# Kernel tuning notes

Measured on AMD Instinct MI355X. Metric: run time of the kernel, lower is better.

## Reference

```python
import jax, jax.numpy as jnp
import numpy as np

DIM = 512
HEADS = 8
DHEAD = 64
B, H, W = 4, 128, 128


def _dwconv(x, k):
    # x: (b, c, h, w), k: (c, 1, 3, 3) depthwise kernel (groups = c)
    return jax.lax.conv_general_dilated(
        x, k, window_strides=(1, 1), padding='SAME',
        dimension_numbers=('NCHW', 'OIHW', 'NCHW'),
        feature_group_count=x.shape[1])


def _l2norm(x, eps=1e-12):
    # torch F.normalize(p=2, dim=-1): x / clamp(||x||, eps)
    n = jnp.sqrt(jnp.sum(x * x, axis=-1, keepdims=True))
    return x / jnp.maximum(n, eps)


def setup_inputs() -> dict:
    key = jax.random.key(0)
    ks = jax.random.split(key, 10)
    s = 0.02
    return {
        'x_in': jax.random.normal(ks[0], (B, H, W, DIM), jnp.float32),
        'illu_fea_trans': jax.random.uniform(ks[1], (B, H, W, DIM), jnp.float32),
        'Wq': jax.random.normal(ks[2], (DIM, DIM), jnp.float32) * s,  # (out,in), no bias
        'Wk': jax.random.normal(ks[3], (DIM, DIM), jnp.float32) * s,
        'Wv': jax.random.normal(ks[4], (DIM, DIM), jnp.float32) * s,
        'rescale': jnp.ones((HEADS, 1, 1), jnp.float32),
        'Wp': jax.random.normal(ks[5], (DIM, DIM), jnp.float32) * s,  # proj weight (out,in)
        'bp': jnp.zeros((DIM,), jnp.float32),
        'pe1': jax.random.normal(ks[6], (DIM, 1, 3, 3), jnp.float32) * s,  # depthwise conv kernels
        'pe2': jax.random.normal(ks[7], (DIM, 1, 3, 3), jnp.float32) * s,
    }


def reference(x_in, illu_fea_trans, Wq, Wk, Wv, rescale, Wp, bp, pe1, pe2):
    b, h, w, c = x_in.shape
    n = h * w
    x = x_in.reshape(b, n, c)
    illu = illu_fea_trans.reshape(b, n, c)

    q = x @ Wq.T
    k = x @ Wk.T
    v = x @ Wv.T

    def to_heads_dn(t):  # (b, n, heads*d) -> (b, heads, d, n)
        return t.reshape(b, n, HEADS, DHEAD).transpose(0, 2, 3, 1)

    illu_h = illu.reshape(b, n, HEADS, DHEAD)
    v = ((v.reshape(b, n, HEADS, DHEAD)) * illu_h).transpose(0, 2, 3, 1)  # (b,heads,d,n)
    q = _l2norm(to_heads_dn(q))  # normalize along n
    k = _l2norm(to_heads_dn(k))

    # channel attention: (b,heads,d,d) score matrix
    attn = jnp.einsum('bhdn,bhen->bhde', k, q) * rescale
    attn = jax.nn.softmax(attn, axis=-1)
    xo = jnp.einsum('bhde,bhen->bhdn', attn, v)  # (b,heads,d,n)

    xo = xo.transpose(0, 3, 1, 2).reshape(b, n, HEADS * DHEAD)  # (b,n,c)
    out_c = (xo @ Wp.T + bp).reshape(b, h, w, c)

    # positional branch: depthwise conv -> GELU -> depthwise conv on v image
    v_img = v.reshape(b, HEADS * DHEAD, h, w)
    p = _dwconv(v_img, pe1)
    p = jax.nn.gelu(p, approximate=False)  # torch F.gelu default = erf
    p = _dwconv(p, pe2)
    out_p = p.transpose(0, 2, 3, 1)

    return out_c + out_p
```

## Files before the change

### kernel.cpp

```cpp
#include <hip/hip_runtime.h>
#include <hip/hip_bf16.h>
#include <math.h>

typedef __bf16 bf16;
typedef __attribute__((ext_vector_type(4))) __bf16 bf16x4;
typedef __attribute__((ext_vector_type(8))) __bf16 bf16x8;
typedef __attribute__((ext_vector_type(4))) float f32x4;

#define GLL(gp, lp) __builtin_amdgcn_global_load_lds( \
    (const __attribute__((address_space(1))) unsigned int*)(gp), \
    (__attribute__((address_space(3))) unsigned int*)(lp), 16, 0, 0)

#define WAIT_LGKM0() do { asm volatile("s_waitcnt lgkmcnt(0)" ::: "memory"); \
                          __builtin_amdgcn_sched_barrier(0); } while (0)
#define WAIT_VMC(n) do { asm volatile("s_waitcnt vmcnt(" #n ")" ::: "memory"); \
                         __builtin_amdgcn_sched_barrier(0); } while (0)
#define BARRIER_FENCE() asm volatile("s_barrier" ::: "memory")


__device__ __forceinline__ bf16x8 cvt8(float4 a, float4 b) {
  bf16x8 o;
  o[0] = (bf16)a.x; o[1] = (bf16)a.y; o[2] = (bf16)a.z; o[3] = (bf16)a.w;
  o[4] = (bf16)b.x; o[5] = (bf16)b.y; o[6] = (bf16)b.z; o[7] = (bf16)b.w;
  return o;
}

__global__ __launch_bounds__(256) void prep_kernel(
    const float* __restrict__ x, const float* __restrict__ Wq,
    const float* __restrict__ Wk, const float* __restrict__ Wv,
    bf16* __restrict__ xb, bf16* __restrict__ wqkv,
    float* __restrict__ zattn, float* __restrict__ ssq, float* __restrict__ ssk)
{
  const long XG = 33554432L / 8;
  const long WG = 262144L / 8;
  long i = (long)blockIdx.x * 256 + threadIdx.x;
  if (i < XG) {
    const float4* xp = (const float4*)x;
    float4 a = xp[i * 2], b = xp[i * 2 + 1];
    *(bf16x8*)(xb + i * 8) = cvt8(a, b);
  } else if (i < XG + 3 * WG) {
    long j = i - XG;
    int w = (int)(j / WG);
    long r = j % WG;
    const float* src = (w == 0) ? Wq : ((w == 1) ? Wk : Wv);
    const float4* sp = (const float4*)src;
    float4 a = sp[r * 2], b = sp[r * 2 + 1];
    *(bf16x8*)(wqkv + (long)w * 262144 + r * 8) = cvt8(a, b);
  } else {
    long j = (i - XG - 3 * WG) * 8;
    float4 z = make_float4(0.f, 0.f, 0.f, 0.f);
    if (j < 131072) {
      *(float4*)(zattn + j) = z; *(float4*)(zattn + j + 4) = z;
    } else if (j < 133120) {
      long r = j - 131072; *(float4*)(ssq + r) = z; *(float4*)(ssq + r + 4) = z;
    } else {
      long r = j - 133120; *(float4*)(ssk + r) = z; *(float4*)(ssk + r + 4) = z;
    }
  }
}

__device__ __forceinline__ void gemm_tile_mainloop(
    const bf16* __restrict__ A, const bf16* __restrict__ B,
    int m0, int n0, bf16* As, bf16* Bs, f32x4 acc[4][4])
{
  int tid = threadIdx.x;
  int lane = tid & 63, wave = tid >> 6;
  int wy = wave >> 1, wx = wave & 1;
  int srow = tid >> 2;
  int scol = ((tid & 3) ^ (srow & 3)) * 8;
  const bf16* ag = A + ((size_t)(m0 + srow) << 9) + scol;
  const bf16* bg = B + ((size_t)(n0 + srow) << 9) + scol;
  bf16* lA = As + wave * 512;
  bf16* lB = Bs + wave * 512;
  int mloc = lane & 15;
  int kq = lane >> 4;

#define STG(t) do { \
    GLL(ag + (t) * 32,         lA + ((t) % 3) * 4096);        \
    GLL(ag + (t) * 32 + 32768, lA + ((t) % 3) * 4096 + 2048); \
    GLL(bg + (t) * 32,         lB + ((t) % 3) * 4096);        \
    GLL(bg + (t) * 32 + 32768, lB + ((t) % 3) * 4096 + 2048); \
  } while (0)

  STG(0);
  STG(1);
  WAIT_VMC(4);
  BARRIER_FENCE();

#pragma unroll
  for (int t = 0; t < 16; ++t) {
    if (t + 2 < 16) STG(t + 2);
    const bf16* Ac = As + (t % 3) * 4096;
    const bf16* Bc = Bs + (t % 3) * 4096;
    bf16x8 af[4], bfr[4];
#pragma unroll
    for (int tt = 0; tt < 4; tt++) {
      int arow = wy * 64 + tt * 16 + mloc;
      af[tt] = *(const bf16x8*)&Ac[arow * 32 + ((kq ^ (arow & 3)) << 3)];
      int brow = wx * 64 + tt * 16 + mloc;
      bfr[tt] = *(const bf16x8*)&Bc[brow * 32 + ((kq ^ (brow & 3)) << 3)];
    }
    WAIT_LGKM0();
    __builtin_amdgcn_s_setprio(1);
#pragma unroll
    for (int ty = 0; ty < 4; ty++)
#pragma unroll
      for (int tx = 0; tx < 4; tx++)
        acc[ty][tx] = __builtin_amdgcn_mfma_f32_16x16x32_bf16(
            af[ty], bfr[tx], acc[ty][tx], 0, 0, 0);
    __builtin_amdgcn_s_setprio(0);
    if (t <= 13)      { WAIT_VMC(4); }
    else if (t == 14) { WAIT_VMC(0); }
    if (t < 15) BARRIER_FENCE();
  }
#undef STG
}

__global__ __launch_bounds__(256, 3) void gemm_qkv_kernel(
    const bf16* __restrict__ xb, const bf16* __restrict__ wqkv,
    const float* __restrict__ illu,
    bf16* __restrict__ qbT, bf16* __restrict__ kbT, bf16* __restrict__ vb,
    float* __restrict__ ssq, float* __restrict__ ssk)
{
  __shared__ __align__(16) bf16 As[12288];
  __shared__ __align__(16) bf16 Bs[12288];
  int bid = blockIdx.x;
  int xcd = bid & 7, s = bid >> 3;
  int mt = xcd * 64 + s / 12, nt = s % 12;
  int m0 = mt * 128, n0 = nt * 128;
  f32x4 acc[4][4] = {};
  gemm_tile_mainloop(xb, wqkv, m0, n0, As, Bs, acc);

  int tid = threadIdx.x, lane = tid & 63, wave = tid >> 6;
  int wy = wave >> 1, wx = wave & 1;
  int r0 = m0 + wy * 64 + ((lane >> 4) << 2);
  int c0 = n0 + wx * 64 + (lane & 15);
  int region = n0 >> 9;
  if (region < 2) {
    bf16* outp = region ? kbT : qbT;
    float* dst = (region ? ssk : ssq) + (m0 >> 14) * 512;
    int bb = r0 >> 14;
    int nl0 = r0 & 16383;
#pragma unroll
    for (int tx = 0; tx < 4; tx++) {
      int lc = (c0 + tx * 16) & 511;
      bf16* colp = outp + (((size_t)bb << 23) + ((size_t)lc << 14));
      float ss = 0.f;
#pragma unroll
      for (int ty = 0; ty < 4; ty++) {
        f32x4 a = acc[ty][tx];
        ss += a[0] * a[0] + a[1] * a[1] + a[2] * a[2] + a[3] * a[3];
        bf16x4 o;
        o[0] = (bf16)a[0]; o[1] = (bf16)a[1]; o[2] = (bf16)a[2]; o[3] = (bf16)a[3];
        *(bf16x4*)&colp[nl0 + ty * 16] = o;
      }
      ss += __shfl_xor(ss, 16);
      ss += __shfl_xor(ss, 32);
      if ((lane >> 4) == 0) atomicAdd(dst + lc, ss);
    }
  } else {
#pragma unroll
    for (int tx = 0; tx < 4; tx++) {
      int lc = (c0 + tx * 16) & 511;
#pragma unroll
      for (int ty = 0; ty < 4; ty++) {
#pragma unroll
        for (int r = 0; r < 4; r++) {
          size_t idx = ((size_t)(r0 + ty * 16 + r) << 9) + lc;
          vb[idx] = (bf16)(acc[ty][tx][r] * illu[idx]);
        }
      }
    }
  }
}

__global__ __launch_bounds__(256) void attn_dots_kernel(
    const bf16* __restrict__ qbT, const bf16* __restrict__ kbT,
    float* __restrict__ attn)
{
  __shared__ __align__(16) bf16 ks[4][4096];
  __shared__ __align__(16) bf16 qs[4][4096];
  int bh = blockIdx.x, sp = blockIdx.y;
  int b = bh >> 3, h = bh & 7;
  int t = threadIdx.x, lane = t & 63, w = t >> 6;
  size_t base = ((size_t)b << 23) + ((size_t)h << 20);
  int n0 = sp * 1024 + w * 256;
  int srow = lane >> 3;
  int scol = ((lane & 7) ^ (srow & 7)) << 3;
  const bf16* kg = kbT + base + (size_t)srow * 16384 + n0 + scol;
  const bf16* qg = qbT + base + (size_t)srow * 16384 + n0 + scol;
  bf16* lk = &ks[w][0];
  bf16* lq = &qs[w][0];
  int mloc = lane & 15, kq = lane >> 4;
  f32x4 acc[4][4] = {};

  for (int it = 0; it < 4; ++it) {
    WAIT_LGKM0();
#pragma unroll
    for (int i = 0; i < 8; ++i) {
      GLL(kg + it * 64 + (size_t)i * 131072, lk + i * 512);
      GLL(qg + it * 64 + (size_t)i * 131072, lq + i * 512);
    }
    WAIT_VMC(0);
    bf16x8 af[4][2], bfq[4][2];
#pragma unroll
    for (int tt = 0; tt < 4; ++tt) {
      int r = tt * 16 + mloc;
#pragma unroll
      for (int kh = 0; kh < 2; ++kh) {
        int slot = (kh * 4 + kq) ^ (r & 7);
        af[tt][kh]  = *(const bf16x8*)&lk[r * 64 + slot * 8];
        bfq[tt][kh] = *(const bf16x8*)&lq[r * 64 + slot * 8];
      }
    }
#pragma unroll
    for (int kh = 0; kh < 2; ++kh)
#pragma unroll
      for (int ta = 0; ta < 4; ++ta)
#pragma unroll
        for (int tb = 0; tb < 4; ++tb)
          acc[ta][tb] = __builtin_amdgcn_mfma_f32_16x16x32_bf16(
              af[ta][kh], bfq[tb][kh], acc[ta][tb], 0, 0, 0);
  }
  float* ap = attn + ((size_t)bh << 12);
  int rr = (lane >> 4) << 2, cc = lane & 15;
#pragma unroll
  for (int ta = 0; ta < 4; ++ta)
#pragma unroll
    for (int tb = 0; tb < 4; ++tb)
#pragma unroll
      for (int r = 0; r < 4; ++r)
        atomicAdd(&ap[(ta * 16 + rr + r) * 64 + tb * 16 + cc], acc[ta][tb][r]);
}

__global__ __launch_bounds__(64) void softmax_kernel(
    float* __restrict__ attn, const float* __restrict__ ssq,
    const float* __restrict__ ssk, const float* __restrict__ rescale)
{
  int bh = blockIdx.x, d = blockIdx.y;
  int b = bh >> 3, h = bh & 7;
  int e = threadIdx.x;
  float nq = fmaxf(sqrtf(ssq[b * 512 + h * 64 + e]), 1e-12f);
  float nk = fmaxf(sqrtf(ssk[b * 512 + h * 64 + d]), 1e-12f);
  float* ap = attn + ((size_t)bh << 12) + d * 64;
  float v = ap[e] * rescale[h] / (nk * nq);
  float m = v;
  for (int o = 32; o > 0; o >>= 1) m = fmaxf(m, __shfl_xor(m, o));
  float ex = expf(v - m);
  float s = ex;
  for (int o = 32; o > 0; o >>= 1) s += __shfl_xor(s, o);
  ap[e] = ex / s;
}

__global__ __launch_bounds__(256) void weff_kernel(
    const float* __restrict__ attn, const float* __restrict__ Wp,
    bf16* __restrict__ wefT)
{
  int cog = blockIdx.x, h = blockIdx.y, b = blockIdx.z;
  __shared__ float at[4096];
  __shared__ float wp[4096];
  int t = threadIdx.x;
  const float* ap = attn + ((size_t)(b * 8 + h) << 12);
  for (int i = t; i < 4096; i += 256) at[i] = ap[i];
  for (int i = t; i < 4096; i += 256) {
    int r = i >> 6, d = i & 63;
    wp[i] = Wp[((size_t)(cog * 64 + r) << 9) + h * 64 + d];
  }
  __syncthreads();
  int co_l = (t & 15) * 4, e_l = (t >> 4) * 4;
  float acc[16] = {0};
  for (int d = 0; d < 64; d++) {
    float w0 = wp[(co_l + 0) * 64 + d];
    float w1 = wp[(co_l + 1) * 64 + d];
    float w2 = wp[(co_l + 2) * 64 + d];
    float w3 = wp[(co_l + 3) * 64 + d];
    float4 av = *(const float4*)&at[d * 64 + e_l];
    acc[0]  += w0 * av.x; acc[1]  += w0 * av.y; acc[2]  += w0 * av.z; acc[3]  += w0 * av.w;
    acc[4]  += w1 * av.x; acc[5]  += w1 * av.y; acc[6]  += w1 * av.z; acc[7]  += w1 * av.w;
    acc[8]  += w2 * av.x; acc[9]  += w2 * av.y; acc[10] += w2 * av.z; acc[11] += w2 * av.w;
    acc[12] += w3 * av.x; acc[13] += w3 * av.y; acc[14] += w3 * av.z; acc[15] += w3 * av.w;
  }
#pragma unroll
  for (int i = 0; i < 4; i++)
#pragma unroll
    for (int j = 0; j < 4; j++)
      wefT[((size_t)b << 18) + ((size_t)(cog * 64 + co_l + i) << 9) + h * 64 + e_l + j] =
          (bf16)acc[i * 4 + j];
}

__global__ __launch_bounds__(256, 3) void gemm_out_kernel(
    const bf16* __restrict__ vb, const bf16* __restrict__ wefT,
    const float* __restrict__ bp, float* __restrict__ out)
{
  __shared__ __align__(16) bf16 As[12288];
  __shared__ __align__(16) bf16 Bs[12288];
  int b = blockIdx.y;
  int bid = blockIdx.x;
  int xcd = bid & 7, s = bid >> 3;
  int mt = xcd * 16 + (s >> 2), nt = s & 3;
  int m0 = mt * 128, n0 = nt * 128;
  const bf16* A = vb + ((size_t)b << 23);
  const bf16* B = wefT + ((size_t)b << 18);
  f32x4 acc[4][4] = {};
  gemm_tile_mainloop(A, B, m0, n0, As, Bs, acc);

  int tid = threadIdx.x, lane = tid & 63, wave = tid >> 6;
  int wy = wave >> 1, wx = wave & 1;
  int r0 = (b << 14) + m0 + wy * 64 + ((lane >> 4) << 2);
  int c0 = n0 + wx * 64 + (lane & 15);
#pragma unroll
  for (int ty = 0; ty < 4; ty++) {
#pragma unroll
    for (int tx = 0; tx < 4; tx++) {
      int lc = c0 + tx * 16;
      float bias = bp[lc];
#pragma unroll
      for (int r = 0; r < 4; r++) {
        int grow = r0 + ty * 16 + r;
        out[((size_t)grow << 9) + lc] = acc[ty][tx][r] + bias;
      }
    }
  }
}

__global__ __launch_bounds__(256) void conv1_kernel(
    const bf16* __restrict__ vb, const float* __restrict__ pe1,
    bf16* __restrict__ pbuf)
{
  int b = blockIdx.y;
  int tile = blockIdx.x;
  int y0 = (tile >> 4) * 8, x0 = (tile & 15) * 8;
  int t = threadIdx.x;
  int cg = (t & 63) * 8, sp0 = t >> 6;
  float w[72];
#pragma unroll
  for (int i = 0; i < 8; i++)
#pragma unroll
    for (int k = 0; k < 9; k++)
      w[i * 9 + k] = pe1[(cg + i) * 9 + k];
  const bf16* vbase = vb + ((size_t)b << 23);
  bf16* pb = pbuf + ((size_t)b << 23);
  for (int s = sp0; s < 64; s += 4) {
    int y = y0 + (s >> 3), x = x0 + (s & 7);
    float a[8] = {0, 0, 0, 0, 0, 0, 0, 0};
#pragma unroll
    for (int ky = 0; ky < 3; ky++) {
      int yy = y + ky - 1;
      if (yy < 0 || yy >= 128) continue;
#pragma unroll
      for (int kx = 0; kx < 3; kx++) {
        int xx = x + kx - 1;
        if (xx < 0 || xx >= 128) continue;
        bf16x8 vv = *(const bf16x8*)&vbase[((size_t)(yy * 128 + xx) << 9) + cg];
#pragma unroll
        for (int i = 0; i < 8; i++) a[i] += (float)vv[i] * w[i * 9 + ky * 3 + kx];
      }
    }
    bf16x8 o;
#pragma unroll
    for (int i = 0; i < 8; i++) {
      float g = 0.5f * a[i] * (1.0f + erff(a[i] * 0.70710678118654752f));
      o[i] = (bf16)g;
    }
    *(bf16x8*)&pb[((size_t)(y * 128 + x) << 9) + cg] = o;
  }
}

__global__ __launch_bounds__(256) void conv2_kernel(
    const bf16* __restrict__ pbuf, const float* __restrict__ pe2,
    float* __restrict__ out)
{
  int b = blockIdx.y;
  int tile = blockIdx.x;
  int y0 = (tile >> 4) * 8, x0 = (tile & 15) * 8;
  int t = threadIdx.x;
  int cg = (t & 63) * 8, sp0 = t >> 6;
  float w[72];
#pragma unroll
  for (int i = 0; i < 8; i++)
#pragma unroll
    for (int k = 0; k < 9; k++)
      w[i * 9 + k] = pe2[(cg + i) * 9 + k];
  const bf16* pb = pbuf + ((size_t)b << 23);
  float* ob = out + ((size_t)b << 23);
  for (int s = sp0; s < 64; s += 4) {
    int y = y0 + (s >> 3), x = x0 + (s & 7);
    float a[8] = {0, 0, 0, 0, 0, 0, 0, 0};
#pragma unroll
    for (int ky = 0; ky < 3; ky++) {
      int yy = y + ky - 1;
      if (yy < 0 || yy >= 128) continue;
#pragma unroll
      for (int kx = 0; kx < 3; kx++) {
        int xx = x + kx - 1;
        if (xx < 0 || xx >= 128) continue;
        bf16x8 vv = *(const bf16x8*)&pb[((size_t)(yy * 128 + xx) << 9) + cg];
#pragma unroll
        for (int i = 0; i < 8; i++) a[i] += (float)vv[i] * w[i * 9 + ky * 3 + kx];
      }
    }
    size_t oi = ((size_t)(y * 128 + x) << 9) + cg;
    float4 o0 = *(float4*)&ob[oi];
    float4 o1 = *(float4*)&ob[oi + 4];
    o0.x += a[0]; o0.y += a[1]; o0.z += a[2]; o0.w += a[3];
    o1.x += a[4]; o1.y += a[5]; o1.z += a[6]; o1.w += a[7];
    *(float4*)&ob[oi] = o0;
    *(float4*)&ob[oi + 4] = o1;
  }
}

extern "C" void kernel_launch(void* const* d_in, const int* in_sizes, int n_in,
                              void* d_out, int out_size, void* d_ws, size_t ws_size,
                              hipStream_t stream) {
  (void)in_sizes; (void)n_in; (void)out_size; (void)ws_size;
  const float* x       = (const float*)d_in[0];
  const float* illu    = (const float*)d_in[1];
  const float* Wq      = (const float*)d_in[2];
  const float* Wk      = (const float*)d_in[3];
  const float* Wv      = (const float*)d_in[4];
  const float* rescale = (const float*)d_in[5];
  const float* Wp      = (const float*)d_in[6];
  const float* bp      = (const float*)d_in[7];
  const float* pe1     = (const float*)d_in[8];
  const float* pe2     = (const float*)d_in[9];
  float* out = (float*)d_out;
  char* ws = (char*)d_ws;

  bf16*  xb   = (bf16*)(ws);
  bf16*  wqkv = (bf16*)(ws + 67108864);
  bf16*  qbT  = (bf16*)(ws + 68681728);
  bf16*  kbT  = (bf16*)(ws + 135790592);
  bf16*  vb   = (bf16*)(ws + 202899456);
  float* ssq  = (float*)(ws + 270008320);
  float* ssk  = (float*)(ws + 270016512);
  float* attn = (float*)(ws + 270024704);
  bf16*  wefT = (bf16*)(ws + 270548992);
  bf16*  pbuf = xb;

  prep_kernel<<<16834, 256, 0, stream>>>(x, Wq, Wk, Wv, xb, wqkv, attn, ssq, ssk);
  gemm_qkv_kernel<<<6144, 256, 0, stream>>>(xb, wqkv, illu, qbT, kbT, vb, ssq, ssk);
  attn_dots_kernel<<<dim3(32, 16), 256, 0, stream>>>(qbT, kbT, attn);
  softmax_kernel<<<dim3(32, 64), 64, 0, stream>>>(attn, ssq, ssk, rescale);
  weff_kernel<<<dim3(8, 8, 4), 256, 0, stream>>>(attn, Wp, wefT);
  gemm_out_kernel<<<dim3(512, 4), 256, 0, stream>>>(vb, wefT, bp, out);
  conv1_kernel<<<dim3(256, 4), 256, 0, stream>>>(vb, pe1, pbuf);
  conv2_kernel<<<dim3(256, 4), 256, 0, stream>>>(pbuf, pe2, out);
}
```

Before: 783.0 us.

## Fuse two depthwise convs via LDS halo tile and change GEMM LDS swizzle

Merges the conv1 (dwconv+GELU) and conv2 kernels into one kernel. Each block computes GELU(conv1) on a 10x10 halo tile for a 128-channel slice, keeps it in shared memory, then applies conv2 from LDS. This removes the round trip of the intermediate bf16 buffer through global memory, at the cost of recomputing halo pixels (about 1.56x conv1 work). It also changes the XOR swizzle in the GEMM mainloop's LDS staging and reads, to use (row>>1)&3 so that LDS bank conflicts drop.

```diff
diff --git a/kernel.cpp b/kernel.cpp
--- a/kernel.cpp
+++ b/kernel.cpp
@@ -67,7 +67,7 @@
   int lane = tid & 63, wave = tid >> 6;
   int wy = wave >> 1, wx = wave & 1;
   int srow = tid >> 2;
-  int scol = ((tid & 3) ^ (srow & 3)) * 8;
+  int scol = ((tid & 3) ^ ((tid >> 3) & 3)) * 8;
   const bf16* ag = A + ((size_t)(m0 + srow) << 9) + scol;
   const bf16* bg = B + ((size_t)(n0 + srow) << 9) + scol;
   bf16* lA = As + wave * 512;
@@ -96,9 +96,9 @@
 #pragma unroll
     for (int tt = 0; tt < 4; tt++) {
       int arow = wy * 64 + tt * 16 + mloc;
-      af[tt] = *(const bf16x8*)&Ac[arow * 32 + ((kq ^ (arow & 3)) << 3)];
+      af[tt] = *(const bf16x8*)&Ac[arow * 32 + ((kq ^ ((arow >> 1) & 3)) << 3)];
       int brow = wx * 64 + tt * 16 + mloc;
-      bfr[tt] = *(const bf16x8*)&Bc[brow * 32 + ((kq ^ (brow & 3)) << 3)];
+      bfr[tt] = *(const bf16x8*)&Bc[brow * 32 + ((kq ^ ((brow >> 1) & 3)) << 3)];
     }
     WAIT_LGKM0();
     __builtin_amdgcn_s_setprio(1);
@@ -323,83 +323,80 @@
   }
 }
 
-__global__ __launch_bounds__(256) void conv1_kernel(
+__global__ __launch_bounds__(256) void conv_fused_kernel(
     const bf16* __restrict__ vb, const float* __restrict__ pe1,
-    bf16* __restrict__ pbuf)
-{
-  int b = blockIdx.y;
+    const float* __restrict__ pe2, float* __restrict__ out)
+{
+  __shared__ __align__(16) bf16 ps[10 * 10 * 128];
+  int b = blockIdx.z;
+  int cs = blockIdx.y;
   int tile = blockIdx.x;
   int y0 = (tile >> 4) * 8, x0 = (tile & 15) * 8;
   int t = threadIdx.x;
-  int cg = (t & 63) * 8, sp0 = t >> 6;
-  float w[72];
+  int cl = (t & 15) * 8;
+  int cg = cs * 128 + cl;
+  int sp = t >> 4;
+  const bf16* vbase = vb + ((size_t)b << 23);
+
+  {
+    float w1[72];
+#pragma unroll
+    for (int i = 0; i < 8; i++)
+#pragma unroll
+      for (int k = 0; k < 9; k++)
+        w1[i * 9 + k] = pe1[(cg + i) * 9 + k];
+    for (int pos = sp; pos < 100; pos += 16) {
+      int py = pos / 10, px = pos % 10;
+      int yy = y0 - 1 + py, xx = x0 - 1 + px;
+      bf16x8 o;
+      if (yy >= 0 && yy < 128 && xx >= 0 && xx < 128) {
+        float a[8] = {0, 0, 0, 0, 0, 0, 0, 0};
+#pragma unroll
+        for (int ky = 0; ky < 3; ky++) {
+          int sy = yy + ky - 1;
+          if (sy < 0 || sy >= 128) continue;
+#pragma unroll
+          for (int kx = 0; kx < 3; kx++) {
+            int sx = xx + kx - 1;
+            if (sx < 0 || sx >= 128) continue;
+            bf16x8 vv = *(const bf16x8*)&vbase[((size_t)(sy * 128 + sx) << 9) + cg];
+#pragma unroll
+            for (int i = 0; i < 8; i++) a[i] += (float)vv[i] * w1[i * 9 + ky * 3 + kx];
+          }
+        }
+#pragma unroll
+        for (int i = 0; i < 8; i++) {
+          float g = 0.5f * a[i] * (1.0f + erff(a[i] * 0.70710678118654752f));
+          o[i] = (bf16)g;
+        }
+      } else {
+#pragma unroll
+        for (int i = 0; i < 8; i++) o[i] = (bf16)0.0f;
+      }
+      *(bf16x8*)&ps[(py * 10 + px) * 128 + cl] = o;
+    }
+  }
+  __syncthreads();
+
+  float w2[72];
 #pragma unroll
   for (int i = 0; i < 8; i++)
 #pragma unroll
     for (int k = 0; k < 9; k++)
-      w[i * 9 + k] = pe1[(cg + i) * 9 + k];
-  const bf16* vbase = vb + ((size_t)b << 23);
-  bf16* pb = pbuf + ((size_t)b << 23);
-  for (int s = sp0; s < 64; s += 4) {
-    int y = y0 + (s >> 3), x = x0 + (s & 7);
+      w2[i * 9 + k] = pe2[(cg + i) * 9 + k];
+  float* ob = out + ((size_t)b << 23);
+  for (int o = sp; o < 64; o += 16) {
+    int oy = o >> 3, ox = o & 7;
     float a[8] = {0, 0, 0, 0, 0, 0, 0, 0};
 #pragma unroll
-    for (int ky = 0; ky < 3; ky++) {
-      int yy = y + ky - 1;
-      if (yy < 0 || yy >= 128) continue;
+    for (int ky = 0; ky < 3; ky++)
 #pragma unroll
       for (int kx = 0; kx < 3; kx++) {
-        int xx = x + kx - 1;
-        if (xx < 0 || xx >= 128) continue;
-        bf16x8 vv = *(const bf16x8*)&vbase[((size_t)(yy * 128 + xx) << 9) + cg];
-#pragma unroll
-        for (int i = 0; i < 8; i++) a[i] += (float)vv[i] * w[i * 9 + ky * 3 + kx];
-      }
-    }
-    bf16x8 o;
-#pragma unroll
-    for (int i = 0; i < 8; i++) {
-      float g = 0.5f * a[i] * (1.0f + erff(a[i] * 0.70710678118654752f));
-      o[i] = (bf16)g;
-    }
-    *(bf16x8*)&pb[((size_t)(y * 128 + x) << 9) + cg] = o;
-  }
-}
-
-__global__ __launch_bounds__(256) void conv2_kernel(
-    const bf16* __restrict__ pbuf, const float* __restrict__ pe2,
-    float* __restrict__ out)
-{
-  int b = blockIdx.y;
-  int tile = blockIdx.x;
-  int y0 = (tile >> 4) * 8, x0 = (tile & 15) * 8;
-  int t = threadIdx.x;
-  int cg = (t & 63) * 8, sp0 = t >> 6;
-  float w[72];
-#pragma unroll
-  for (int i = 0; i < 8; i++)
-#pragma unroll
-    for (int k = 0; k < 9; k++)
-      w[i * 9 + k] = pe2[(cg + i) * 9 + k];
-  const bf16* pb = pbuf + ((size_t)b << 23);
-  float* ob = out + ((size_t)b << 23);
-  for (int s = sp0; s < 64; s += 4) {
-    int y = y0 + (s >> 3), x = x0 + (s & 7);
-    float a[8] = {0, 0, 0, 0, 0, 0, 0, 0};
-#pragma unroll
-    for (int ky = 0; ky < 3; ky++) {
-      int yy = y + ky - 1;
-      if (yy < 0 || yy >= 128) continue;
-#pragma unroll
-      for (int kx = 0; kx < 3; kx++) {
-        int xx = x + kx - 1;
-        if (xx < 0 || xx >= 128) continue;
-        bf16x8 vv = *(const bf16x8*)&pb[((size_t)(yy * 128 + xx) << 9) + cg];
-#pragma unroll
-        for (int i = 0; i < 8; i++) a[i] += (float)vv[i] * w[i * 9 + ky * 3 + kx];
-      }
-    }
-    size_t oi = ((size_t)(y * 128 + x) << 9) + cg;
+        bf16x8 pv = *(const bf16x8*)&ps[((oy + ky) * 10 + (ox + kx)) * 128 + cl];
+#pragma unroll
+        for (int i = 0; i < 8; i++) a[i] += (float)pv[i] * w2[i * 9 + ky * 3 + kx];
+      }
+    size_t oi = ((size_t)((y0 + oy) * 128 + (x0 + ox)) << 9) + cg;
     float4 o0 = *(float4*)&ob[oi];
     float4 o1 = *(float4*)&ob[oi + 4];
     o0.x += a[0]; o0.y += a[1]; o0.z += a[2]; o0.w += a[3];
@@ -435,7 +432,6 @@
   float* ssk  = (float*)(ws + 270016512);
   float* attn = (float*)(ws + 270024704);
   bf16*  wefT = (bf16*)(ws + 270548992);
-  bf16*  pbuf = xb;
 
   prep_kernel<<<16834, 256, 0, stream>>>(x, Wq, Wk, Wv, xb, wqkv, attn, ssq, ssk);
   gemm_qkv_kernel<<<6144, 256, 0, stream>>>(xb, wqkv, illu, qbT, kbT, vb, ssq, ssk);
@@ -443,6 +439,5 @@
   softmax_kernel<<<dim3(32, 64), 64, 0, stream>>>(attn, ssq, ssk, rescale);
   weff_kernel<<<dim3(8, 8, 4), 256, 0, stream>>>(attn, Wp, wefT);
   gemm_out_kernel<<<dim3(512, 4), 256, 0, stream>>>(vb, wefT, bp, out);
-  conv1_kernel<<<dim3(256, 4), 256, 0, stream>>>(vb, pe1, pbuf);
-  conv2_kernel<<<dim3(256, 4), 256, 0, stream>>>(pbuf, pe2, out);
-}
+  conv_fused_kernel<<<dim3(256, 4, 4), 256, 0, stream>>>(vb, pe1, pe2, out);
+}
```

Measured after the change: 741.5 us. 1.06x faster.
